# Optimization experiments

Measured on AMD Instinct MI355X. Metric: run time of the kernel, lower is better.

The kernel has to match this reference:

```python
import jax, jax.numpy as jnp
import numpy as np

B, L, N, M, E_EDGE, C = 8, 256, 1024, 8, 16384, 50
EMB, D, TDIM, ETYPES = 768, 256, 50, 50
H, DH, LAYERS = 4, 64, 2
VOCAB_W, VOCAB_E = 30000, 100000
K_SPLIT = N // 2  # fixed kg/logic node split (original uses data-dependent index)


def setup_inputs() -> dict:
    key = jax.random.key(0)
    ks = jax.random.split(key, 32)
    s = 0.02
    inp = {}
    inp["sentence"] = jax.random.randint(ks[0], (B, L), 0, VOCAB_W)
    inp["mask"] = jnp.ones((B, L), jnp.float32)
    inp["nodes"] = jax.random.randint(ks[1], (B, N, M), 0, VOCAB_E)
    inp["node_mask"] = jnp.ones((B, N, M), jnp.float32)
    inp["node_types"] = jax.random.randint(ks[2], (B, N + 1), 0, 100)
    inp["edges"] = jax.random.randint(ks[3], (B, 2, E_EDGE), 0, N + 1)
    inp["edge_types"] = jax.random.randint(ks[4], (B, E_EDGE), 0, ETYPES)
    inp["word_embed"] = jax.random.normal(ks[5], (VOCAB_W, EMB)) * s
    inp["entity_table"] = jax.random.normal(ks[6], (VOCAB_E, EMB)) * s
    inp["type_table"] = jax.random.normal(ks[7], (100, TDIM)) * s
    inp["mlp_w1"] = jax.random.normal(ks[8], (EMB, 1024)) * s
    inp["mlp_b1"] = jnp.zeros((1024,), jnp.float32)
    inp["mlp_w2"] = jax.random.normal(ks[9], (1024, EMB)) * s
    inp["mlp_b2"] = jnp.zeros((EMB,), jnp.float32)
    inp["ntw_w"] = jax.random.normal(ks[10], (EMB, EMB)) * s
    inp["proj_w"] = jax.random.normal(ks[11], (EMB, D)) * s
    inp["proj_b"] = jnp.zeros((D,), jnp.float32)
    inp["type_proj_w"] = jax.random.normal(ks[12], (TDIM, D)) * s
    inp["edge_type_table"] = jax.random.normal(ks[13], (ETYPES, TDIM)) * s
    inp["gnn_wq"] = jax.random.normal(ks[14], (LAYERS, D, D)) * s
    inp["gnn_wk"] = jax.random.normal(ks[15], (LAYERS, D, D)) * s
    inp["gnn_wv"] = jax.random.normal(ks[16], (LAYERS, D, D)) * s
    inp["gnn_we"] = jax.random.normal(ks[17], (LAYERS, TDIM, D)) * s
    inp["cls_w"] = jax.random.normal(ks[18], (EMB + 2 * D, EMB)) * s
    inp["cls_b"] = jnp.zeros((EMB,), jnp.float32)
    inp["cls2_w"] = jax.random.normal(ks[19], (C, EMB)) * s
    inp["cls2_b"] = jnp.zeros((C,), jnp.float32)
    return inp


def reference(sentence, mask, nodes, node_mask, node_types, edges, edge_types,
              word_embed, entity_table, type_table, mlp_w1, mlp_b1, mlp_w2, mlp_b2,
              ntw_w, proj_w, proj_b, type_proj_w, edge_type_table,
              gnn_wq, gnn_wk, gnn_wv, gnn_we, cls_w, cls_b, cls2_w, cls2_b):
    # PLM encoder stand-in: masked mean pool over word embeddings -> [B, EMB]
    text_vec = (word_embed[sentence] * mask[:, :, None]).sum(1) / (mask.sum(1, keepdims=True) + 1e-9)

    def per_graph(nd, nm, nt, eg, et, tv):
        ne = entity_table[nd]                                        # [N, M, EMB]
        logic = jnp.maximum(ne[K_SPLIT:] @ mlp_w1 + mlp_b1, 0.0) @ mlp_w2 + mlp_b2
        ne = jnp.concatenate([ne[:K_SPLIT], logic], axis=0)
        ne = ne @ ntw_w                                              # x @ W (no bias, no transpose)
        ne = (ne * nm[:, :, None]).sum(axis=1)                       # masked sum pool -> [N, EMB]
        h = jnp.concatenate([tv[None], ne], axis=0) @ proj_w + proj_b  # [N+1, D]
        h = h + type_table[nt] @ type_proj_w                         # inject node-type embeds
        src, dst = eg[0], eg[1]
        eemb = edge_type_table[et]                                   # [E, TDIM]
        Nn = N + 1
        for l in range(LAYERS):
            q = (h @ gnn_wq[l]).reshape(Nn, H, DH)
            k = (h @ gnn_wk[l]).reshape(Nn, H, DH)
            v = (h @ gnn_wv[l]).reshape(Nn, H, DH)
            ke = (eemb @ gnn_we[l]).reshape(E_EDGE, H, DH)
            logits = (q[dst] * (k[src] + ke)).sum(-1) / np.float32(np.sqrt(DH))  # [E, H]
            mx = jax.ops.segment_max(logits, dst, num_segments=Nn)
            ex = jnp.exp(logits - mx[dst])
            den = jax.ops.segment_sum(ex, dst, num_segments=Nn)
            alpha = ex / (den[dst] + 1e-9)
            agg = jax.ops.segment_sum(alpha[..., None] * v[src], dst, num_segments=Nn).reshape(Nn, D)
            h = jax.nn.relu(h + agg)
        return h[0], h[1:1 + C]

    ctx, lab = jax.vmap(per_graph)(nodes, node_mask, node_types, edges, edge_types, text_vec)
    ans_t = jnp.broadcast_to(ctx[:, None, :], (B, C, D))
    prompt = jnp.broadcast_to(text_vec[:, None, :], (B, C, EMB))
    pool = jnp.concatenate([ans_t, lab, prompt], axis=2) @ cls_w + cls_b   # [B, C, EMB]
    return (pool * cls2_w[None]).sum(-1) + cls2_b[None]                     # [B, C]
```

## Files before the change

### kernel.cpp

```cpp
#include <hip/hip_runtime.h>
#include <hip/hip_bf16.h>
#include <stdint.h>

using bf16 = __hip_bfloat16;
typedef __attribute__((ext_vector_type(8))) short short8;
typedef __attribute__((ext_vector_type(4))) float f32x4;
typedef __attribute__((address_space(3))) unsigned int lds_u32;
typedef const __attribute__((address_space(1))) unsigned int gbl_u32;

#define HSTRIDE 1040
#define NNODES 1025
#define EE 16384
#define MAXDEG 192

__device__ __forceinline__ bf16 f2b(float x) { return __float2bfloat16(x); }
__device__ __forceinline__ float b2f(bf16 x) { return __bfloat162float(x); }
__device__ __forceinline__ float bu2f(unsigned short u) {
    union { unsigned int i; float f; } x;
    x.i = ((unsigned int)u) << 16;
    return x.f;
}

__device__ __forceinline__ size_t midx(int row) {
    int G = row >> 3, m = row & 7, b = G >> 9;
    return (size_t)(G + 512 * (b + 1)) * 8 + m;
}

__global__ __launch_bounds__(256) void k_transpose_cvt(const float* __restrict__ in,
                                                       bf16* __restrict__ out, int R, int C) {
    __shared__ float tile[32][33];
    int bx = blockIdx.x * 32;
    int by = blockIdx.y * 32;
    int tx = threadIdx.x, ty = threadIdx.y;
    for (int i = 0; i < 32; i += 8)
        tile[ty + i][tx] = in[(size_t)(by + ty + i) * C + bx + tx];
    __syncthreads();
    for (int i = 0; i < 32; i += 8)
        out[(size_t)(bx + ty + i) * R + by + tx] = f2b(tile[tx][ty + i]);
}

__global__ __launch_bounds__(256) void k_transpose_qkv(const float* __restrict__ wq,
                                                       const float* __restrict__ wk,
                                                       const float* __restrict__ wv,
                                                       bf16* __restrict__ out) {
    __shared__ float tile[32][33];
    int z = blockIdx.z;
    int l = z / 3, which = z % 3;
    const float* in = (which == 0 ? wq : which == 1 ? wk : wv) + (size_t)l * 65536;
    bf16* o = out + (size_t)l * 196608 + (size_t)which * 65536;
    int bx = blockIdx.x * 32;
    int by = blockIdx.y * 32;
    int tx = threadIdx.x, ty = threadIdx.y;
    for (int i = 0; i < 32; i += 8)
        tile[ty + i][tx] = in[(size_t)(by + ty + i) * 256 + bx + tx];
    __syncthreads();
    for (int i = 0; i < 32; i += 8)
        o[(size_t)(bx + ty + i) * 256 + by + tx] = f2b(tile[tx][ty + i]);
}

__global__ __launch_bounds__(256) void k_small3(const float* __restrict__ type_table,
                                                const float* __restrict__ type_proj_w,
                                                const float* __restrict__ edge_tt,
                                                const float* __restrict__ gnn_we,
                                                float* __restrict__ tpe,
                                                float* __restrict__ etewe) {
    int r = blockIdx.x, c = threadIdx.x;
    const float* X;
    const float* W;
    float* out;
    if (r < 100) {
        X = type_table + r * 50; W = type_proj_w; out = tpe + r * 256;
    } else if (r < 150) {
        X = edge_tt + (r - 100) * 50; W = gnn_we; out = etewe + (r - 100) * 256;
    } else {
        X = edge_tt + (r - 150) * 50; W = gnn_we + 12800; out = etewe + 12800 + (r - 150) * 256;
    }
    float acc = 0.f;
    for (int k = 0; k < 50; k++) acc += X[k] * W[k * 256 + c];
    out[c] = acc;
}

__global__ __launch_bounds__(256) void k_weff(const float* __restrict__ cls_w,
                                              const float* __restrict__ cls2_w,
                                              const float* __restrict__ cls_b,
                                              const float* __restrict__ cls2_b,
                                              float* __restrict__ weff,
                                              float* __restrict__ beff) {
    int c = blockIdx.y;
    int wave = threadIdx.x >> 6, lane = threadIdx.x & 63;
    int k = blockIdx.x * 4 + wave;
    float acc = 0.f;
    for (int e = lane; e < 768; e += 64)
        acc += cls_w[(size_t)k * 768 + e] * cls2_w[c * 768 + e];
    for (int s = 32; s > 0; s >>= 1) acc += __shfl_xor(acc, s, 64);
    if (lane == 0) weff[c * 1280 + k] = acc;
    if (blockIdx.x == 0 && wave == 0) {
        float bacc = 0.f;
        for (int e = lane; e < 768; e += 64) bacc += cls_b[e] * cls2_w[c * 768 + e];
        for (int s = 32; s > 0; s >>= 1) bacc += __shfl_xor(bacc, s, 64);
        if (lane == 0) beff[c] = bacc + cls2_b[c];
    }
}

__global__ __launch_bounds__(256) void k_textvec_part(const int* __restrict__ sent,
                                                      const float* __restrict__ mask,
                                                      const float* __restrict__ we,
                                                      float* __restrict__ tvp,
                                                      float* __restrict__ msump) {
    int b = blockIdx.x, ch = blockIdx.y, tid = threadIdx.x;
    float a0 = 0.f, a1 = 0.f, a2 = 0.f, ms = 0.f;
    for (int l = ch * 32; l < ch * 32 + 32; l++) {
        int w = sent[b * 256 + l];
        float mm = mask[b * 256 + l];
        const float* row = we + (size_t)w * 768;
        a0 += mm * row[tid];
        a1 += mm * row[tid + 256];
        a2 += mm * row[tid + 512];
        ms += mm;
    }
    float* dst = tvp + (size_t)(b * 8 + ch) * 768;
    dst[tid] = a0;
    dst[tid + 256] = a1;
    dst[tid + 512] = a2;
    if (tid == 0) msump[b * 8 + ch] = ms;
}

__global__ __launch_bounds__(256) void k_tvred(const float* __restrict__ tvp,
                                               const float* __restrict__ msump,
                                               float* __restrict__ tv) {
    int b = blockIdx.x, tid = threadIdx.x;
    float ms = 0.f;
    for (int p = 0; p < 8; p++) ms += msump[b * 8 + p];
    float inv = 1.f / (ms + 1e-9f);
    float a0 = 0.f, a1 = 0.f, a2 = 0.f;
    for (int p = 0; p < 8; p++) {
        const float* s = tvp + (size_t)(b * 8 + p) * 768;
        a0 += s[tid];
        a1 += s[tid + 256];
        a2 += s[tid + 512];
    }
    tv[b * 768 + tid] = a0 * inv;
    tv[b * 768 + tid + 256] = a1 * inv;
    tv[b * 768 + tid + 512] = a2 * inv;
}

__global__ __launch_bounds__(256) void gemm_mlp1(const int* __restrict__ nodes,
                                                 const float* __restrict__ ent,
                                                 const bf16* __restrict__ Bt,
                                                 const float* __restrict__ b1,
                                                 const float* __restrict__ node_mask,
                                                 bf16* __restrict__ pooledh) {
    __shared__ bf16 As[128][32];
    __shared__ bf16 Bs[128][32];
    const int tid = threadIdx.x;
    const int bid = blockIdx.x;
    const int j = bid >> 3;
    const int m0 = (((bid & 7) * 32) + (j >> 3)) << 7;
    const int n0 = (j & 7) << 7;
    const int lane = tid & 63;
    const int wave = tid >> 6;
    const int wm = (wave >> 1) << 6;
    const int wn = (wave & 1) << 6;
    const int rsel = lane & 15;
    const int qd = lane >> 4;
    const int K = 768;

    const float* arow[4];
    int rl_row = tid >> 3;
    int piece4 = (tid & 7) << 2;
#pragma unroll
    for (int p = 0; p < 4; p++) {
        int grow = m0 + p * 32 + rl_row;
        int id = nodes[midx(grow)];
        arow[p] = ent + (size_t)id * 768 + piece4;
    }

    f32x4 acc[4][4];
#pragma unroll
    for (int i = 0; i < 4; i++)
#pragma unroll
        for (int jj = 0; jj < 4; jj++) acc[i][jj] = (f32x4){0.f, 0.f, 0.f, 0.f};

    const int c0 = tid, r0 = c0 >> 2, kk0 = (c0 & 3) << 3;
    const int c1 = tid + 256, r1 = c1 >> 2, kk1 = (c1 & 3) << 3;

    for (int k0 = 0; k0 < K; k0 += 32) {
        __syncthreads();
        const bf16* gb0 = Bt + (size_t)(n0 + r0) * K + (k0 + kk0);
        __builtin_amdgcn_global_load_lds((gbl_u32*)gb0, (lds_u32*)&Bs[r0][kk0], 16, 0, 0);
        const bf16* gb1 = Bt + (size_t)(n0 + r1) * K + (k0 + kk1);
        __builtin_amdgcn_global_load_lds((gbl_u32*)gb1, (lds_u32*)&Bs[r1][kk1], 16, 0, 0);
#pragma unroll
        for (int p = 0; p < 4; p++) {
            float4 v = *(const float4*)(arow[p] + k0);
            union { bf16 h[4]; uint2 u; } pk;
            pk.h[0] = f2b(v.x); pk.h[1] = f2b(v.y); pk.h[2] = f2b(v.z); pk.h[3] = f2b(v.w);
            *(uint2*)&As[p * 32 + rl_row][piece4] = pk.u;
        }
        __syncthreads();
        short8 af[4], bfr[4];
#pragma unroll
        for (int i = 0; i < 4; i++) af[i] = *(const short8*)&As[wm + i * 16 + rsel][qd << 3];
#pragma unroll
        for (int jj = 0; jj < 4; jj++) bfr[jj] = *(const short8*)&Bs[wn + jj * 16 + rsel][qd << 3];
#pragma unroll
        for (int i = 0; i < 4; i++)
#pragma unroll
            for (int jj = 0; jj < 4; jj++)
                acc[i][jj] = __builtin_amdgcn_mfma_f32_16x16x32_bf16(af[i], bfr[jj], acc[i][jj], 0, 0, 0);
    }
#pragma unroll
    for (int i = 0; i < 4; i++) {
        const int rbase = m0 + wm + i * 16 + (qd << 2);
        float w4[4];
#pragma unroll
        for (int r = 0; r < 4; r++) w4[r] = node_mask[midx(rbase + r)];
        const int Gout = (m0 + wm + i * 16 + ((qd & 2) << 2)) >> 3;
#pragma unroll
        for (int jj = 0; jj < 4; jj++) {
            const int col = n0 + wn + jj * 16 + rsel;
            const float bv = b1[col];
            float s = 0.f;
#pragma unroll
            for (int r = 0; r < 4; r++) s += w4[r] * fmaxf(acc[i][jj][r] + bv, 0.f);
            s += __shfl_xor(s, 16, 64);
            if ((qd & 1) == 0) pooledh[(size_t)Gout * 1024 + col] = f2b(s);
        }
    }
}

__global__ __launch_bounds__(256) void k_summask(const float* __restrict__ node_mask,
                                                 float* __restrict__ summask) {
    int G = blockIdx.x * 256 + threadIdx.x;
    if (G >= 4096) return;
    int b = G >> 9;
    const float* p = node_mask + (size_t)(G + 512 * (b + 1)) * 8;
    float s = 0.f;
    for (int m = 0; m < 8; m++) s += p[m];
    summask[G] = s;
}

template <int EPIL>
__global__ __launch_bounds__(256) void gemm_bt(const bf16* __restrict__ A,
                                               const bf16* __restrict__ Bt,
                                               bf16* __restrict__ Cb, float* __restrict__ Cf,
                                               const float* __restrict__ bias,
                                               const float* __restrict__ smr,
                                               int M, int N, int K, int NT, int swz) {
    __shared__ bf16 As[128][32];
    __shared__ bf16 Bs[128][32];
    const int tid = threadIdx.x;
    const int bid = blockIdx.x;
    int mt, nt;
    if (swz) {
        const int MT8 = (M >> 7) >> 3;
        const int j = bid >> 3;
        mt = (bid & 7) * MT8 + j / NT;
        nt = j - (j / NT) * NT;
    } else {
        mt = bid / NT;
        nt = bid - mt * NT;
    }
    const int m0 = mt << 7;
    const int n0 = nt << 7;
    const int lane = tid & 63;
    const int wave = tid >> 6;
    const int wm = (wave >> 1) << 6;
    const int wn = (wave & 1) << 6;
    const int rsel = lane & 15;
    const int qd = lane >> 4;
    f32x4 acc[4][4];
#pragma unroll
    for (int i = 0; i < 4; i++)
#pragma unroll
        for (int jj = 0; jj < 4; jj++) acc[i][jj] = (f32x4){0.f, 0.f, 0.f, 0.f};
// ... 35 lines not shown
        }
#pragma unroll
        for (int jj = 0; jj < 4; jj++) {
            const int col = n0 + wn + jj * 16 + rsel;
            float bv = 0.f;
            if constexpr (EPIL == 4 || EPIL == 5) bv = bias[col];
#pragma unroll
            for (int r = 0; r < 4; r++) {
                const int row = rbase + r;
                if constexpr (EPIL == 0) {
                    Cb[(size_t)row * N + col] = f2b(acc[i][jj][r]);
                } else if constexpr (EPIL == 4) {
                    const int bb = row >> 10, nn2 = row & 1023;
                    Cf[((size_t)bb * HSTRIDE + 1 + nn2) * 256 + col] = acc[i][jj][r] + bv;
                } else {
                    const int dest = row + 512 * ((row >> 9) + 1);
                    Cb[(size_t)dest * N + col] = f2b(acc[i][jj][r] + sm4[r] * bv);
                }
            }
        }
    }
}

__global__ __launch_bounds__(256) void k_pool_kg(const int* __restrict__ nodes,
                                                 const float* __restrict__ nmask,
                                                 const float* __restrict__ ent,
                                                 bf16* __restrict__ pooled) {
    int bid = blockIdx.x;
    int b = bid >> 9, n = bid & 511;
    int tid = threadIdx.x;
    int base = (((b << 10) + n) << 3);
    float a0 = 0.f, a1 = 0.f, a2 = 0.f;
    for (int m = 0; m < 8; m++) {
        float w = nmask[base + m];
        const float* row = ent + (size_t)nodes[base + m] * 768;
        a0 += w * row[tid];
        a1 += w * row[tid + 256];
        a2 += w * row[tid + 512];
    }
    bf16* dst = pooled + (size_t)((b << 10) + n) * 768;
    dst[tid] = f2b(a0);
    dst[tid + 256] = f2b(a1);
    dst[tid + 512] = f2b(a2);
}

__global__ __launch_bounds__(256) void k_tpe_add(const int* __restrict__ ntypes,
                                                 const float* __restrict__ tpe,
                                                 const float* __restrict__ tv,
                                                 const float* __restrict__ proj_w,
                                                 const float* __restrict__ proj_b,
                                                 float* __restrict__ h, bf16* __restrict__ hbf) {
    int i = blockIdx.x;
    int b = blockIdx.y;
    int c = threadIdx.x;
    size_t idx = ((size_t)b * HSTRIDE + i) * 256 + c;
    if (i < NNODES) {
        int t = ntypes[b * NNODES + i];
        float v;
        if (i == 0) {
            v = proj_b[c];
            for (int k = 0; k < 768; k++) v += tv[b * 768 + k] * proj_w[k * 256 + c];
        } else {
            v = h[idx];
        }
        v += tpe[t * 256 + c];
        h[idx] = v;
        hbf[idx] = f2b(v);
    } else {
        h[idx] = 0.f;
        hbf[idx] = f2b(0.f);
    }
}

__global__ void k_zero(int* p, int n) {
    int i = blockIdx.x * 256 + threadIdx.x;
    if (i < n) p[i] = 0;
}

__global__ __launch_bounds__(256) void k_count(const int* __restrict__ edges,
                                               int* __restrict__ counts) {
    int flat = blockIdx.x * 256 + threadIdx.x;
    int b = flat >> 14, e = flat & (EE - 1);
    int d = edges[b * 2 * EE + EE + e];
    atomicAdd(&counts[b * NNODES + d], 1);
}

__global__ __launch_bounds__(256) void k_scan(const int* __restrict__ counts,
                                              int* __restrict__ offs, int* __restrict__ cursor) {
    int b = blockIdx.x, t = threadIdx.x;
    __shared__ int tsum[256];
    int beg = t * 5;
    int end = beg + 5;
    if (end > NNODES) end = NNODES;
    int cl[5];
    int s = 0;
    for (int i = beg; i < end; i++) {
        int v = counts[b * NNODES + i];
        cl[i - beg] = v;
        s += v;
    }
    tsum[t] = s;
    __syncthreads();
    for (int d = 1; d < 256; d <<= 1) {
        int v = tsum[t];
        int vo = (t >= d) ? tsum[t - d] : 0;
        __syncthreads();
        tsum[t] = v + vo;
        __syncthreads();
    }
    int run = (t == 0) ? 0 : tsum[t - 1];
    for (int i = beg; i < end; i++) {
        offs[b * 1026 + i] = run;
        cursor[b * NNODES + i] = run;
        run += cl[i - beg];
    }
    if (beg == NNODES) offs[b * 1026 + NNODES] = run;
}

__global__ __launch_bounds__(256) void k_scatter(const int* __restrict__ edges,
                                                 int* __restrict__ cursor, int* __restrict__ eord) {
    int flat = blockIdx.x * 256 + threadIdx.x;
    int b = flat >> 14, e = flat & (EE - 1);
    int d = edges[b * 2 * EE + EE + e];
    int pos = atomicAdd(&cursor[b * NNODES + d], 1);
    eord[b * EE + pos] = e;
}

__global__ __launch_bounds__(256) void k_gnn_node(const int* __restrict__ edges,
                                                  const int* __restrict__ etypes,
                                                  const int* __restrict__ offs,
                                                  const int* __restrict__ eord,
                                                  const float* __restrict__ etewe,
                                                  const bf16* __restrict__ qkv,
                                                  float* __restrict__ h, bf16* __restrict__ hbf) {
    int bid = blockIdx.x;
    int b = bid / NNODES, n = bid % NNODES;
    int o0 = offs[b * 1026 + n];
    int deg = offs[b * 1026 + n + 1] - o0;
    if (deg > MAXDEG) deg = MAXDEG;
    int tid = threadIdx.x, lane = tid & 63, wave = tid >> 6;
    __shared__ float qs[256];
    __shared__ float elog[MAXDEG][4];
    __shared__ int srcs[MAXDEG];
    __shared__ float smax[4], sden[4];
    __shared__ float vpart[4][256];
    size_t qbase = ((size_t)(b * HSTRIDE + n)) * 768;
    qs[tid] = b2f(qkv[qbase + tid]);
    __syncthreads();
// ... 19 lines not shown
    __syncthreads();
    if (deg > 0) {
        int hh = wave;
        float m = -1e30f;
        for (int i = lane; i < deg; i += 64) m = fmaxf(m, elog[i][hh]);
        for (int s = 32; s > 0; s >>= 1) m = fmaxf(m, __shfl_xor(m, s, 64));
        float den = 0.f;
        for (int i = lane; i < deg; i += 64) den += expf(elog[i][hh] - m);
        for (int s = 32; s > 0; s >>= 1) den += __shfl_xor(den, s, 64);
        if (lane == 0) { smax[hh] = m; sden[hh] = den; }
    }
    __syncthreads();
    for (int i = tid; i < deg; i += 256) {
#pragma unroll
        for (int hh = 0; hh < 4; hh++)
            elog[i][hh] = expf(elog[i][hh] - smax[hh]) / (sden[hh] + 1e-9f);
    }
    __syncthreads();
    float a0 = 0.f, a1 = 0.f, a2 = 0.f, a3 = 0.f;
    const int hsel = lane >> 4;
    for (int i = wave; i < deg; i += 4) {
        float w = elog[i][hsel];
        const bf16* vrow = qkv + ((size_t)(b * HSTRIDE + srcs[i])) * 768 + 512 + lane * 4;
        ushort4 u = *reinterpret_cast<const ushort4*>(vrow);
        a0 += w * bu2f(u.x);
        a1 += w * bu2f(u.y);
        a2 += w * bu2f(u.z);
        a3 += w * bu2f(u.w);
    }
    vpart[wave][lane * 4 + 0] = a0;
    vpart[wave][lane * 4 + 1] = a1;
    vpart[wave][lane * 4 + 2] = a2;
    vpart[wave][lane * 4 + 3] = a3;
    __syncthreads();
    float acc = vpart[0][tid] + vpart[1][tid] + vpart[2][tid] + vpart[3][tid];
    size_t hidx = ((size_t)(b * HSTRIDE + n)) * 256 + tid;
    float v = fmaxf(h[hidx] + acc, 0.f);
    h[hidx] = v;
    hbf[hidx] = f2b(v);
}

__global__ __launch_bounds__(256) void k_cls(const float* __restrict__ h,
                                             const float* __restrict__ tv,
                                             const float* __restrict__ weff,
                                             const float* __restrict__ beff,
                                             float* __restrict__ out) {
    int bc = blockIdx.x;
    int b = bc / 50, c = bc % 50;
    int tid = threadIdx.x;
    const float* we = weff + c * 1280;
    float acc = 0.f;
// ... 35 lines not shown
    const float* ntw_w        = (const float*)d_in[14];
    const float* proj_w       = (const float*)d_in[15];
    const float* proj_b       = (const float*)d_in[16];
    const float* type_proj_w  = (const float*)d_in[17];
    const float* edge_tt      = (const float*)d_in[18];
    const float* gnn_wq       = (const float*)d_in[19];
    const float* gnn_wk       = (const float*)d_in[20];
    const float* gnn_wv       = (const float*)d_in[21];
    const float* gnn_we       = (const float*)d_in[22];
    const float* cls_w        = (const float*)d_in[23];
    const float* cls_b        = (const float*)d_in[24];
    const float* cls2_w       = (const float*)d_in[25];
    const float* cls2_b       = (const float*)d_in[26];

    char* ws = (char*)d_ws;
    size_t off = 0;
    auto alloc = [&](size_t bytes) {
        size_t r = off;
        off += (bytes + 255) & ~((size_t)255);
        return r;
    };
    bf16* w1t     = (bf16*)(ws + alloc((size_t)1024 * 768 * 2));
    bf16* w2t     = (bf16*)(ws + alloc((size_t)768 * 1024 * 2));
    bf16* ntwt    = (bf16*)(ws + alloc((size_t)768 * 768 * 2));
    bf16* projt   = (bf16*)(ws + alloc((size_t)256 * 768 * 2));
    bf16* wqkvt   = (bf16*)(ws + alloc((size_t)2 * 768 * 256 * 2));
    float* tpe    = (float*)(ws + alloc((size_t)100 * 256 * 4));
    float* etewe  = (float*)(ws + alloc((size_t)2 * 50 * 256 * 4));
    float* weff   = (float*)(ws + alloc((size_t)50 * 1280 * 4));
    float* beff   = (float*)(ws + alloc(256));
    float* tv     = (float*)(ws + alloc((size_t)8 * 768 * 4));
    float* tvp    = (float*)(ws + alloc((size_t)64 * 768 * 4));
    float* msump  = (float*)(ws + alloc((size_t)64 * 4));
    float* summask= (float*)(ws + alloc((size_t)4096 * 4));
    int* counts   = (int*)(ws + alloc((size_t)8 * NNODES * 4));
    int* offs     = (int*)(ws + alloc((size_t)8 * 1026 * 4));
    int* cursor   = (int*)(ws + alloc((size_t)8 * NNODES * 4));
    int* eord     = (int*)(ws + alloc((size_t)8 * EE * 4));
    bf16* pooledh = (bf16*)(ws + alloc((size_t)4096 * 1024 * 2));
    bf16* pooled  = (bf16*)(ws + alloc((size_t)8192 * 768 * 2));
    bf16* ne2     = (bf16*)(ws + alloc((size_t)8192 * 768 * 2));
    float* h      = (float*)(ws + alloc((size_t)8 * HSTRIDE * 256 * 4));
    bf16* hbf     = (bf16*)(ws + alloc((size_t)8 * HSTRIDE * 256 * 2));
    bf16* qkv     = (bf16*)(ws + alloc((size_t)8 * HSTRIDE * 768 * 2));

    dim3 tb(32, 8);
    k_transpose_cvt<<<dim3(32, 24), tb, 0, stream>>>(mlp_w1, w1t, 768, 1024);
    k_transpose_cvt<<<dim3(24, 32), tb, 0, stream>>>(mlp_w2, w2t, 1024, 768);
    k_transpose_cvt<<<dim3(24, 24), tb, 0, stream>>>(ntw_w, ntwt, 768, 768);
    k_transpose_cvt<<<dim3(8, 24), tb, 0, stream>>>(proj_w, projt, 768, 256);
    k_transpose_qkv<<<dim3(8, 8, 6), tb, 0, stream>>>(gnn_wq, gnn_wk, gnn_wv, wqkvt);
    k_small3<<<200, 256, 0, stream>>>(type_table, type_proj_w, edge_tt, gnn_we, tpe, etewe);
    k_weff<<<dim3(320, 50), 256, 0, stream>>>(cls_w, cls2_w, cls_b, cls2_b, weff, beff);
    k_textvec_part<<<dim3(8, 8), 256, 0, stream>>>(sentence, mask, word_embed, tvp, msump);
    k_tvred<<<8, 256, 0, stream>>>(tvp, msump, tv);

    gemm_mlp1<<<2048, 256, 0, stream>>>(nodes, entity_table, w1t, mlp_b1, node_mask, pooledh);
    k_summask<<<16, 256, 0, stream>>>(node_mask, summask);
    gemm_bt<5><<<192, 256, 0, stream>>>(pooledh, w2t, pooled, nullptr, mlp_b2, summask, 4096, 768, 1024, 6, 1);
    k_pool_kg<<<4096, 256, 0, stream>>>(nodes, node_mask, entity_table, pooled);
    gemm_bt<0><<<384, 256, 0, stream>>>(pooled, ntwt, ne2, nullptr, nullptr, nullptr, 8192, 768, 768, 6, 1);
    gemm_bt<4><<<128, 256, 0, stream>>>(ne2, projt, nullptr, h, proj_b, nullptr, 8192, 256, 768, 2, 1);
    k_tpe_add<<<dim3(1040, 8), 256, 0, stream>>>(node_types, tpe, tv, proj_w, proj_b, h, hbf);

    k_zero<<<(8 * NNODES + 255) / 256, 256, 0, stream>>>(counts, 8 * NNODES);
    k_count<<<512, 256, 0, stream>>>(edges, counts);
    k_scan<<<8, 256, 0, stream>>>(counts, offs, cursor);
    k_scatter<<<512, 256, 0, stream>>>(edges, cursor, eord);

    for (int l = 0; l < 2; l++) {
        gemm_bt<0><<<390, 256, 0, stream>>>(hbf, wqkvt + l * 196608, qkv, nullptr, nullptr, nullptr, 8320, 768, 256, 6, 0);
        k_gnn_node<<<8 * NNODES, 256, 0, stream>>>(edges, edge_types, offs, eord,
                                                   etewe + l * 12800, qkv, h, hbf);
    }
    k_cls<<<400, 256, 0, stream>>>(h, tv, weff, beff, (float*)d_out);
}
```

Measured before the change: 870.4 us.

## Merge prep kernels into mega-launches and fold ntw into proj weight

Replaces about 17 small launches (weight transposes, table projections, text-vector reduction, edge counting, scan and scatter) with a few multi-role kernels that dispatch on block index. The two chained GEMMs (pooled@ntw then @proj) are precomputed as one combined 768x256 weight, removing the 8192x768x768 GEMM and its intermediate buffer. The text-vector projection is split into partial sums reduced in k_tpe_add. This cuts launch overhead and FLOPs. The cost is heterogeneous blocks inside each launch, plus a small rounding change from multiplying the weights before casting to bf16.

```diff
diff --git a/kernel.cpp b/kernel.cpp
--- a/kernel.cpp
+++ b/kernel.cpp
@@ -26,231 +26,15 @@
     return (size_t)(G + 512 * (b + 1)) * 8 + m;
 }
 
-__global__ __launch_bounds__(256) void k_transpose_cvt(const float* __restrict__ in,
-                                                       bf16* __restrict__ out, int R, int C) {
-    __shared__ float tile[32][33];
-    int bx = blockIdx.x * 32;
-    int by = blockIdx.y * 32;
-    int tx = threadIdx.x, ty = threadIdx.y;
-    for (int i = 0; i < 32; i += 8)
-        tile[ty + i][tx] = in[(size_t)(by + ty + i) * C + bx + tx];
-    __syncthreads();
-    for (int i = 0; i < 32; i += 8)
-        out[(size_t)(bx + ty + i) * R + by + tx] = f2b(tile[tx][ty + i]);
-}
-
-__global__ __launch_bounds__(256) void k_transpose_qkv(const float* __restrict__ wq,
-                                                       const float* __restrict__ wk,
-                                                       const float* __restrict__ wv,
-                                                       bf16* __restrict__ out) {
-    __shared__ float tile[32][33];
-    int z = blockIdx.z;
-    int l = z / 3, which = z % 3;
-    const float* in = (which == 0 ? wq : which == 1 ? wk : wv) + (size_t)l * 65536;
-    bf16* o = out + (size_t)l * 196608 + (size_t)which * 65536;
-    int bx = blockIdx.x * 32;
-    int by = blockIdx.y * 32;
-    int tx = threadIdx.x, ty = threadIdx.y;
-    for (int i = 0; i < 32; i += 8)
-        tile[ty + i][tx] = in[(size_t)(by + ty + i) * 256 + bx + tx];
-    __syncthreads();
-    for (int i = 0; i < 32; i += 8)
-        o[(size_t)(bx + ty + i) * 256 + by + tx] = f2b(tile[tx][ty + i]);
-}
-
-__global__ __launch_bounds__(256) void k_small3(const float* __restrict__ type_table,
-                                                const float* __restrict__ type_proj_w,
-                                                const float* __restrict__ edge_tt,
-                                                const float* __restrict__ gnn_we,
-                                                float* __restrict__ tpe,
-                                                float* __restrict__ etewe) {
-    int r = blockIdx.x, c = threadIdx.x;
-    const float* X;
-    const float* W;
-    float* out;
-    if (r < 100) {
-        X = type_table + r * 50; W = type_proj_w; out = tpe + r * 256;
-    } else if (r < 150) {
-        X = edge_tt + (r - 100) * 50; W = gnn_we; out = etewe + (r - 100) * 256;
-    } else {
-        X = edge_tt + (r - 150) * 50; W = gnn_we + 12800; out = etewe + 12800 + (r - 150) * 256;
-    }
-    float acc = 0.f;
-    for (int k = 0; k < 50; k++) acc += X[k] * W[k * 256 + c];
-    out[c] = acc;
-}
-
-__global__ __launch_bounds__(256) void k_weff(const float* __restrict__ cls_w,
-                                              const float* __restrict__ cls2_w,
-                                              const float* __restrict__ cls_b,
-                                              const float* __restrict__ cls2_b,
-                                              float* __restrict__ weff,
-                                              float* __restrict__ beff) {
-    int c = blockIdx.y;
-    int wave = threadIdx.x >> 6, lane = threadIdx.x & 63;
-    int k = blockIdx.x * 4 + wave;
-    float acc = 0.f;
-    for (int e = lane; e < 768; e += 64)
-        acc += cls_w[(size_t)k * 768 + e] * cls2_w[c * 768 + e];
-    for (int s = 32; s > 0; s >>= 1) acc += __shfl_xor(acc, s, 64);
-    if (lane == 0) weff[c * 1280 + k] = acc;
-    if (blockIdx.x == 0 && wave == 0) {
-        float bacc = 0.f;
-        for (int e = lane; e < 768; e += 64) bacc += cls_b[e] * cls2_w[c * 768 + e];
-        for (int s = 32; s > 0; s >>= 1) bacc += __shfl_xor(bacc, s, 64);
-        if (lane == 0) beff[c] = bacc + cls2_b[c];
-    }
-}
-
-__global__ __launch_bounds__(256) void k_textvec_part(const int* __restrict__ sent,
-                                                      const float* __restrict__ mask,
-                                                      const float* __restrict__ we,
-                                                      float* __restrict__ tvp,
-                                                      float* __restrict__ msump) {
-    int b = blockIdx.x, ch = blockIdx.y, tid = threadIdx.x;
-    float a0 = 0.f, a1 = 0.f, a2 = 0.f, ms = 0.f;
-    for (int l = ch * 32; l < ch * 32 + 32; l++) {
-        int w = sent[b * 256 + l];
-        float mm = mask[b * 256 + l];
-        const float* row = we + (size_t)w * 768;
-        a0 += mm * row[tid];
-        a1 += mm * row[tid + 256];
-        a2 += mm * row[tid + 512];
-        ms += mm;
-    }
-    float* dst = tvp + (size_t)(b * 8 + ch) * 768;
-    dst[tid] = a0;
-    dst[tid + 256] = a1;
-    dst[tid + 512] = a2;
-    if (tid == 0) msump[b * 8 + ch] = ms;
-}
-
-__global__ __launch_bounds__(256) void k_tvred(const float* __restrict__ tvp,
-                                               const float* __restrict__ msump,
-                                               float* __restrict__ tv) {
-    int b = blockIdx.x, tid = threadIdx.x;
-    float ms = 0.f;
-    for (int p = 0; p < 8; p++) ms += msump[b * 8 + p];
-    float inv = 1.f / (ms + 1e-9f);
-    float a0 = 0.f, a1 = 0.f, a2 = 0.f;
-    for (int p = 0; p < 8; p++) {
-        const float* s = tvp + (size_t)(b * 8 + p) * 768;
-        a0 += s[tid];
-        a1 += s[tid + 256];
-        a2 += s[tid + 512];
-    }
-    tv[b * 768 + tid] = a0 * inv;
-    tv[b * 768 + tid + 256] = a1 * inv;
-    tv[b * 768 + tid + 512] = a2 * inv;
-}
-
-__global__ __launch_bounds__(256) void gemm_mlp1(const int* __restrict__ nodes,
-                                                 const float* __restrict__ ent,
-                                                 const bf16* __restrict__ Bt,
-                                                 const float* __restrict__ b1,
-                                                 const float* __restrict__ node_mask,
-                                                 bf16* __restrict__ pooledh) {
+template <int EPIL>
+__device__ __forceinline__ void gemm_body(const bf16* __restrict__ A, const bf16* __restrict__ Bt,
+                                          bf16* __restrict__ Cb, float* __restrict__ Cf,
+                                          const float* __restrict__ bias,
+                                          const float* __restrict__ smr,
+                                          int M, int N, int K, int NT, int swz, int bid) {
     __shared__ bf16 As[128][32];
     __shared__ bf16 Bs[128][32];
     const int tid = threadIdx.x;
-    const int bid = blockIdx.x;
-    const int j = bid >> 3;
-    const int m0 = (((bid & 7) * 32) + (j >> 3)) << 7;
-    const int n0 = (j & 7) << 7;
-    const int lane = tid & 63;
-    const int wave = tid >> 6;
-    const int wm = (wave >> 1) << 6;
-    const int wn = (wave & 1) << 6;
-    const int rsel = lane & 15;
-    const int qd = lane >> 4;
-    const int K = 768;
-
-    const float* arow[4];
-    int rl_row = tid >> 3;
-    int piece4 = (tid & 7) << 2;
-#pragma unroll
-    for (int p = 0; p < 4; p++) {
-        int grow = m0 + p * 32 + rl_row;
-        int id = nodes[midx(grow)];
-        arow[p] = ent + (size_t)id * 768 + piece4;
-    }
-
-    f32x4 acc[4][4];
-#pragma unroll
-    for (int i = 0; i < 4; i++)
-#pragma unroll
-        for (int jj = 0; jj < 4; jj++) acc[i][jj] = (f32x4){0.f, 0.f, 0.f, 0.f};
-
-    const int c0 = tid, r0 = c0 >> 2, kk0 = (c0 & 3) << 3;
-    const int c1 = tid + 256, r1 = c1 >> 2, kk1 = (c1 & 3) << 3;
-
-    for (int k0 = 0; k0 < K; k0 += 32) {
-        __syncthreads();
-        const bf16* gb0 = Bt + (size_t)(n0 + r0) * K + (k0 + kk0);
-        __builtin_amdgcn_global_load_lds((gbl_u32*)gb0, (lds_u32*)&Bs[r0][kk0], 16, 0, 0);
-        const bf16* gb1 = Bt + (size_t)(n0 + r1) * K + (k0 + kk1);
-        __builtin_amdgcn_global_load_lds((gbl_u32*)gb1, (lds_u32*)&Bs[r1][kk1], 16, 0, 0);
-#pragma unroll
-        for (int p = 0; p < 4; p++) {
-            float4 v = *(const float4*)(arow[p] + k0);
-            union { bf16 h[4]; uint2 u; } pk;
-            pk.h[0] = f2b(v.x); pk.h[1] = f2b(v.y); pk.h[2] = f2b(v.z); pk.h[3] = f2b(v.w);
-            *(uint2*)&As[p * 32 + rl_row][piece4] = pk.u;
-        }
-        __syncthreads();
-        short8 af[4], bfr[4];
-#pragma unroll
-        for (int i = 0; i < 4; i++) af[i] = *(const short8*)&As[wm + i * 16 + rsel][qd << 3];
-#pragma unroll
-        for (int jj = 0; jj < 4; jj++) bfr[jj] = *(const short8*)&Bs[wn + jj * 16 + rsel][qd << 3];
-#pragma unroll
-        for (int i = 0; i < 4; i++)
-#pragma unroll
-            for (int jj = 0; jj < 4; jj++)
-                acc[i][jj] = __builtin_amdgcn_mfma_f32_16x16x32_bf16(af[i], bfr[jj], acc[i][jj], 0, 0, 0);
-    }
-#pragma unroll
-    for (int i = 0; i < 4; i++) {
-        const int rbase = m0 + wm + i * 16 + (qd << 2);
-        float w4[4];
-#pragma unroll
-        for (int r = 0; r < 4; r++) w4[r] = node_mask[midx(rbase + r)];
-        const int Gout = (m0 + wm + i * 16 + ((qd & 2) << 2)) >> 3;
-#pragma unroll
-        for (int jj = 0; jj < 4; jj++) {
-            const int col = n0 + wn + jj * 16 + rsel;
-            const float bv = b1[col];
-            float s = 0.f;
-#pragma unroll
-            for (int r = 0; r < 4; r++) s += w4[r] * fmaxf(acc[i][jj][r] + bv, 0.f);
-            s += __shfl_xor(s, 16, 64);
-            if ((qd & 1) == 0) pooledh[(size_t)Gout * 1024 + col] = f2b(s);
-        }
-    }
-}
-
-__global__ __launch_bounds__(256) void k_summask(const float* __restrict__ node_mask,
-                                                 float* __restrict__ summask) {
-    int G = blockIdx.x * 256 + threadIdx.x;
-    if (G >= 4096) return;
-    int b = G >> 9;
-    const float* p = node_mask + (size_t)(G + 512 * (b + 1)) * 8;
-    float s = 0.f;
-    for (int m = 0; m < 8; m++) s += p[m];
-    summask[G] = s;
-}
-
-template <int EPIL>
-__global__ __launch_bounds__(256) void gemm_bt(const bf16* __restrict__ A,
-                                               const bf16* __restrict__ Bt,
-                                               bf16* __restrict__ Cb, float* __restrict__ Cf,
-                                               const float* __restrict__ bias,
-                                               const float* __restrict__ smr,
-                                               int M, int N, int K, int NT, int swz) {
-    __shared__ bf16 As[128][32];
-    __shared__ bf16 Bs[128][32];
-    const int tid = threadIdx.x;
-    const int bid = blockIdx.x;
     int mt, nt;
     if (swz) {
         const int MT8 = (M >> 7) >> 3;
@@ -332,32 +116,380 @@
     }
 }
 
-__global__ __launch_bounds__(256) void k_pool_kg(const int* __restrict__ nodes,
-                                                 const float* __restrict__ nmask,
-                                                 const float* __restrict__ ent,
-                                                 bf16* __restrict__ pooled) {
-    int bid = blockIdx.x;
-    int b = bid >> 9, n = bid & 511;
+template <int EPIL>
+__global__ __launch_bounds__(256) void gemm_bt(const bf16* __restrict__ A,
+                                               const bf16* __restrict__ Bt,
+                                               bf16* __restrict__ Cb, float* __restrict__ Cf,
+                                               const float* __restrict__ bias,
+                                               const float* __restrict__ smr,
+                                               int M, int N, int K, int NT, int swz) {
+    gemm_body<EPIL>(A, Bt, Cb, Cf, bias, smr, M, N, K, NT, swz, blockIdx.x);
+}
+
+__device__ __forceinline__ void tr_tile(const float* __restrict__ in, bf16* __restrict__ out,
+                                        int R, int C, int gx, int gy, int tid,
+                                        float (*tile)[33]) {
+    int tx = tid & 31, ty = tid >> 5;
+    int bx = gx * 32, by = gy * 32;
+    for (int i = 0; i < 32; i += 8)
+        tile[ty + i][tx] = in[(size_t)(by + ty + i) * C + bx + tx];
+    __syncthreads();
+    for (int i = 0; i < 32; i += 8)
+        out[(size_t)(bx + ty + i) * R + by + tx] = f2b(tile[tx][ty + i]);
+}
+
+__global__ __launch_bounds__(256) void k_prep(
+    const float* __restrict__ mlp_w1, const float* __restrict__ mlp_w2,
+    const float* __restrict__ ntw_w, const float* __restrict__ proj_w,
+    const float* __restrict__ gnn_wq, const float* __restrict__ gnn_wk,
+    const float* __restrict__ gnn_wv,
+    const float* __restrict__ type_table, const float* __restrict__ type_proj_w,
+    const float* __restrict__ edge_tt, const float* __restrict__ gnn_we,
+    const float* __restrict__ cls_w, const float* __restrict__ cls2_w,
+    const float* __restrict__ cls_b, const float* __restrict__ cls2_b,
+    const int* __restrict__ sent, const float* __restrict__ maskp,
+    const float* __restrict__ we,
+    bf16* __restrict__ w1t, bf16* __restrict__ w2t, bf16* __restrict__ ntwbf,
+    bf16* __restrict__ projt, bf16* __restrict__ wqkvt,
+    float* __restrict__ tpe, float* __restrict__ etewe,
+    float* __restrict__ weff, float* __restrict__ beff,
+    float* __restrict__ tvp, float* __restrict__ msump, int* __restrict__ counts) {
+    __shared__ float tile[32][33];
+    int u = blockIdx.x;
     int tid = threadIdx.x;
-    int base = (((b << 10) + n) << 3);
-    float a0 = 0.f, a1 = 0.f, a2 = 0.f;
-    for (int m = 0; m < 8; m++) {
-        float w = nmask[base + m];
-        const float* row = ent + (size_t)nodes[base + m] * 768;
-        a0 += w * row[tid];
-        a1 += w * row[tid + 256];
-        a2 += w * row[tid + 512];
-    }
-    bf16* dst = pooled + (size_t)((b << 10) + n) * 768;
-    dst[tid] = f2b(a0);
-    dst[tid + 256] = f2b(a1);
-    dst[tid + 512] = f2b(a2);
+    if (u < 768) {
+        tr_tile(mlp_w1, w1t, 768, 1024, u % 32, u / 32, tid, tile);
+        return;
+    }
+    u -= 768;
+    if (u < 768) {
+        tr_tile(mlp_w2, w2t, 1024, 768, u % 24, u / 24, tid, tile);
+        return;
+    }
+    u -= 768;
+    if (u < 576) {
+        int base = (u * 256 + tid) * 4;
+        float4 v = *(const float4*)(ntw_w + base);
+        union { bf16 h[4]; uint2 q; } pk;
+        pk.h[0] = f2b(v.x); pk.h[1] = f2b(v.y); pk.h[2] = f2b(v.z); pk.h[3] = f2b(v.w);
+        *(uint2*)(ntwbf + base) = pk.q;
+        return;
+    }
+    u -= 576;
+    if (u < 192) {
+        tr_tile(proj_w, projt, 768, 256, u % 8, u / 8, tid, tile);
+        return;
+    }
+    u -= 192;
+    if (u < 384) {
+        int z = u / 64, v = u % 64;
+        int l = z / 3, which = z % 3;
+        const float* in = (which == 0 ? gnn_wq : which == 1 ? gnn_wk : gnn_wv) + (size_t)l * 65536;
+        bf16* o = wqkvt + (size_t)l * 196608 + (size_t)which * 65536;
+        tr_tile(in, o, 256, 256, v % 8, v / 8, tid, tile);
+        return;
+    }
+    u -= 384;
+    if (u < 200) {
+        const float* X;
+        const float* W;
+        float* out;
+        if (u < 100) {
+            X = type_table + u * 50; W = type_proj_w; out = tpe + u * 256;
+        } else if (u < 150) {
+            X = edge_tt + (u - 100) * 50; W = gnn_we; out = etewe + (u - 100) * 256;
+        } else {
+            X = edge_tt + (u - 150) * 50; W = gnn_we + 12800; out = etewe + 12800 + (u - 150) * 256;
+        }
+        float acc = 0.f;
+        for (int k = 0; k < 50; k++) acc += X[k] * W[k * 256 + tid];
+        out[tid] = acc;
+        return;
+    }
+    u -= 200;
+    if (u < 320) {
+        int wave = tid >> 6, lane = tid & 63;
+        int k = u * 4 + wave;
+        float wrow[12];
+#pragma unroll
+        for (int t = 0; t < 12; t++) wrow[t] = cls_w[(size_t)k * 768 + t * 64 + lane];
+        for (int c = 0; c < 50; c++) {
+            const float* c2 = cls2_w + c * 768;
+            float acc = 0.f;
+#pragma unroll
+            for (int t = 0; t < 12; t++) acc += wrow[t] * c2[t * 64 + lane];
+            for (int s = 32; s > 0; s >>= 1) acc += __shfl_xor(acc, s, 64);
+            if (lane == 0) weff[c * 1280 + k] = acc;
+        }
+        if (u == 0) {
+            float brow[12];
+#pragma unroll
+            for (int t = 0; t < 12; t++) brow[t] = cls_b[t * 64 + lane];
+            for (int c = wave; c < 50; c += 4) {
+                const float* c2 = cls2_w + c * 768;
+                float acc = 0.f;
+#pragma unroll
+                for (int t = 0; t < 12; t++) acc += brow[t] * c2[t * 64 + lane];
+                for (int s = 32; s > 0; s >>= 1) acc += __shfl_xor(acc, s, 64);
+                if (lane == 0) beff[c] = acc + cls2_b[c];
+            }
+        }
+        return;
+    }
+    u -= 320;
+    if (u < 64) {
+        int b = u >> 3, ch = u & 7;
+        float a0 = 0.f, a1 = 0.f, a2 = 0.f, ms = 0.f;
+        for (int l = ch * 32; l < ch * 32 + 32; l++) {
+            int w = sent[b * 256 + l];
+            float mm = maskp[b * 256 + l];
+            const float* row = we + (size_t)w * 768;
+            a0 += mm * row[tid];
+            a1 += mm * row[tid + 256];
+            a2 += mm * row[tid + 512];
+            ms += mm;
+        }
+        float* dst = tvp + (size_t)(b * 8 + ch) * 768;
+        dst[tid] = a0;
+        dst[tid + 256] = a1;
+        dst[tid + 512] = a2;
+        if (tid == 0) msump[b * 8 + ch] = ms;
+        return;
+    }
+    u -= 64;
+    {
+        int i = u * 256 + tid;
+        if (i < 8 * NNODES) counts[i] = 0;
+    }
+}
+
+__global__ __launch_bounds__(256) void k_mid(
+    const bf16* __restrict__ projt, const bf16* __restrict__ ntwbf, bf16* __restrict__ wnpt,
+    const float* __restrict__ tvp, const float* __restrict__ msump, float* __restrict__ tv,
+    const float* __restrict__ node_mask, float* __restrict__ summask,
+    const int* __restrict__ edges, int* __restrict__ counts) {
+    int u = blockIdx.x;
+    int tid = threadIdx.x;
+    if (u < 12) {
+        gemm_body<0>(projt, ntwbf, wnpt, nullptr, nullptr, nullptr, 256, 768, 768, 6, 0, u);
+        return;
+    }
+    u -= 12;
+    if (u < 8) {
+        int b = u;
+        float ms = 0.f;
+        for (int p = 0; p < 8; p++) ms += msump[b * 8 + p];
+        float inv = 1.f / (ms + 1e-9f);
+        float a0 = 0.f, a1 = 0.f, a2 = 0.f;
+        for (int p = 0; p < 8; p++) {
+            const float* s = tvp + (size_t)(b * 8 + p) * 768;
+            a0 += s[tid];
+            a1 += s[tid + 256];
+            a2 += s[tid + 512];
+        }
+        tv[b * 768 + tid] = a0 * inv;
+        tv[b * 768 + tid + 256] = a1 * inv;
+        tv[b * 768 + tid + 512] = a2 * inv;
+        return;
+    }
+    u -= 8;
+    if (u < 16) {
+        int G = u * 256 + tid;
+        if (G < 4096) {
+            int b = G >> 9;
+            const float* p = node_mask + (size_t)(G + 512 * (b + 1)) * 8;
+            float s = 0.f;
+            for (int m = 0; m < 8; m++) s += p[m];
+            summask[G] = s;
+        }
+        return;
+    }
+    u -= 16;
+    {
+        int flat = u * 256 + tid;
+        int b = flat >> 14, e = flat & (EE - 1);
+        int d = edges[b * 2 * EE + EE + e];
+        atomicAdd(&counts[b * NNODES + d], 1);
+    }
+}
+
+__global__ __launch_bounds__(256) void k_mlp1_scan(
+    const int* __restrict__ nodes, const float* __restrict__ ent,
+    const bf16* __restrict__ Bt, const float* __restrict__ b1,
+    const float* __restrict__ node_mask, bf16* __restrict__ pooledh,
+    const int* __restrict__ counts, int* __restrict__ offs, int* __restrict__ cursor) {
+    __shared__ bf16 As[128][32];
+    __shared__ bf16 Bs[128][32];
+    __shared__ int tsum[256];
+    const int tid = threadIdx.x;
+    const int bid = blockIdx.x;
+    if (bid >= 2048) {
+        int b = bid - 2048, t = tid;
+        int beg = t * 5;
+        int end = beg + 5;
+        if (end > NNODES) end = NNODES;
+        int cl[5];
+        int s = 0;
+        for (int i = beg; i < end; i++) {
+            int v = counts[b * NNODES + i];
+            cl[i - beg] = v;
+            s += v;
+        }
+        tsum[t] = s;
+        __syncthreads();
+        for (int d = 1; d < 256; d <<= 1) {
+            int v = tsum[t];
+            int vo = (t >= d) ? tsum[t - d] : 0;
+            __syncthreads();
+            tsum[t] = v + vo;
+            __syncthreads();
+        }
+        int run = (t == 0) ? 0 : tsum[t - 1];
+        for (int i = beg; i < end; i++) {
+            offs[b * 1026 + i] = run;
+            cursor[b * NNODES + i] = run;
+            run += cl[i - beg];
+        }
+        if (beg == NNODES) offs[b * 1026 + NNODES] = run;
+        return;
+    }
+    const int j = bid >> 3;
+    const int m0 = (((bid & 7) * 32) + (j >> 3)) << 7;
+    const int n0 = (j & 7) << 7;
+    const int lane = tid & 63;
+    const int wave = tid >> 6;
+    const int wm = (wave >> 1) << 6;
+    const int wn = (wave & 1) << 6;
+    const int rsel = lane & 15;
+    const int qd = lane >> 4;
+    const int K = 768;
+
+    const float* arow[4];
+    int rl_row = tid >> 3;
+    int piece4 = (tid & 7) << 2;
+#pragma unroll
+    for (int p = 0; p < 4; p++) {
+        int grow = m0 + p * 32 + rl_row;
+        int id = nodes[midx(grow)];
+        arow[p] = ent + (size_t)id * 768 + piece4;
+    }
+
+    f32x4 acc[4][4];
+#pragma unroll
+    for (int i = 0; i < 4; i++)
+#pragma unroll
+        for (int jj = 0; jj < 4; jj++) acc[i][jj] = (f32x4){0.f, 0.f, 0.f, 0.f};
+
+    const int c0 = tid, r0 = c0 >> 2, kk0 = (c0 & 3) << 3;
+    const int c1 = tid + 256, r1 = c1 >> 2, kk1 = (c1 & 3) << 3;
+
+    for (int k0 = 0; k0 < K; k0 += 32) {
+        __syncthreads();
+        const bf16* gb0 = Bt + (size_t)(n0 + r0) * K + (k0 + kk0);
+        __builtin_amdgcn_global_load_lds((gbl_u32*)gb0, (lds_u32*)&Bs[r0][kk0], 16, 0, 0);
+        const bf16* gb1 = Bt + (size_t)(n0 + r1) * K + (k0 + kk1);
+        __builtin_amdgcn_global_load_lds((gbl_u32*)gb1, (lds_u32*)&Bs[r1][kk1], 16, 0, 0);
+#pragma unroll
+        for (int p = 0; p < 4; p++) {
+            float4 v = *(const float4*)(arow[p] + k0);
+            union { bf16 h[4]; uint2 u; } pk;
+            pk.h[0] = f2b(v.x); pk.h[1] = f2b(v.y); pk.h[2] = f2b(v.z); pk.h[3] = f2b(v.w);
+            *(uint2*)&As[p * 32 + rl_row][piece4] = pk.u;
+        }
+        __syncthreads();
+        short8 af[4], bfr[4];
+#pragma unroll
+        for (int i = 0; i < 4; i++) af[i] = *(const short8*)&As[wm + i * 16 + rsel][qd << 3];
+#pragma unroll
+        for (int jj = 0; jj < 4; jj++) bfr[jj] = *(const short8*)&Bs[wn + jj * 16 + rsel][qd << 3];
+#pragma unroll
+        for (int i = 0; i < 4; i++)
+#pragma unroll
+            for (int jj = 0; jj < 4; jj++)
+                acc[i][jj] = __builtin_amdgcn_mfma_f32_16x16x32_bf16(af[i], bfr[jj], acc[i][jj], 0, 0, 0);
+    }
+#pragma unroll
+    for (int i = 0; i < 4; i++) {
+        const int rbase = m0 + wm + i * 16 + (qd << 2);
+        float w4[4];
+#pragma unroll
+        for (int r = 0; r < 4; r++) w4[r] = node_mask[midx(rbase + r)];
+        const int Gout = (m0 + wm + i * 16 + ((qd & 2) << 2)) >> 3;
+#pragma unroll
+        for (int jj = 0; jj < 4; jj++) {
+            const int col = n0 + wn + jj * 16 + rsel;
+            const float bv = b1[col];
+            float s = 0.f;
+#pragma unroll
+            for (int r = 0; r < 4; r++) s += w4[r] * fmaxf(acc[i][jj][r] + bv, 0.f);
+            s += __shfl_xor(s, 16, 64);
+            if ((qd & 1) == 0) pooledh[(size_t)Gout * 1024 + col] = f2b(s);
+        }
+    }
+}
+
+__global__ __launch_bounds__(256) void k_mega4(
+    const bf16* __restrict__ pooledh, const bf16* __restrict__ w2t, bf16* __restrict__ pooled,
+    const float* __restrict__ mlp_b2, const float* __restrict__ summask,
+    const int* __restrict__ nodes, const float* __restrict__ nmask, const float* __restrict__ ent,
+    const float* __restrict__ tv, const float* __restrict__ proj_w, float* __restrict__ hp) {
+    int u = blockIdx.x;
+    int tid = threadIdx.x;
+    if (u < 192) {
+        gemm_body<5>(pooledh, w2t, pooled, nullptr, mlp_b2, summask, 4096, 768, 1024, 6, 1, u);
+        return;
+    }
+    u -= 192;
+    if (u < 4096) {
+        int b = u >> 9, n = u & 511;
+        int base = (((b << 10) + n) << 3);
+        float a0 = 0.f, a1 = 0.f, a2 = 0.f;
+        for (int m = 0; m < 8; m++) {
+            float w = nmask[base + m];
+            const float* row = ent + (size_t)nodes[base + m] * 768;
+            a0 += w * row[tid];
+            a1 += w * row[tid + 256];
+            a2 += w * row[tid + 512];
+        }
+        bf16* dst = pooled + (size_t)((b << 10) + n) * 768;
+        dst[tid] = f2b(a0);
+        dst[tid + 256] = f2b(a1);
+        dst[tid + 512] = f2b(a2);
+        return;
+    }
+    u -= 4096;
+    {
+        int b = u / 6, kc = u % 6;
+        float acc = 0.f;
+        for (int k = kc * 128; k < kc * 128 + 128; k++)
+            acc += tv[b * 768 + k] * proj_w[k * 256 + tid];
+        hp[(size_t)(b * 6 + kc) * 256 + tid] = acc;
+    }
+}
+
+__global__ __launch_bounds__(256) void k_mega5(
+    const bf16* __restrict__ pooled, const bf16* __restrict__ wnpt,
+    float* __restrict__ h, const float* __restrict__ proj_b,
+    const int* __restrict__ edges, int* __restrict__ cursor, int* __restrict__ eord) {
+    int u = blockIdx.x;
+    int tid = threadIdx.x;
+    if (u < 128) {
+        gemm_body<4>(pooled, wnpt, nullptr, h, proj_b, nullptr, 8192, 256, 768, 2, 1, u);
+        return;
+    }
+    u -= 128;
+    {
+        int flat = u * 256 + tid;
+        int b = flat >> 14, e = flat & (EE - 1);
+        int d = edges[b * 2 * EE + EE + e];
+        int pos = atomicAdd(&cursor[b * NNODES + d], 1);
+        eord[b * EE + pos] = e;
+    }
 }
 
 __global__ __launch_bounds__(256) void k_tpe_add(const int* __restrict__ ntypes,
                                                  const float* __restrict__ tpe,
-                                                 const float* __restrict__ tv,
-                                                 const float* __restrict__ proj_w,
+                                                 const float* __restrict__ hp,
                                                  const float* __restrict__ proj_b,
                                                  float* __restrict__ h, bf16* __restrict__ hbf) {
     int i = blockIdx.x;
@@ -369,7 +501,7 @@
         float v;
         if (i == 0) {
             v = proj_b[c];
-            for (int k = 0; k < 768; k++) v += tv[b * 768 + k] * proj_w[k * 256 + c];
+            for (int p = 0; p < 6; p++) v += hp[(size_t)(b * 6 + p) * 256 + c];
         } else {
             v = h[idx];
         }
@@ -380,60 +512,6 @@
         h[idx] = 0.f;
         hbf[idx] = f2b(0.f);
     }
-}
-
-__global__ void k_zero(int* p, int n) {
-    int i = blockIdx.x * 256 + threadIdx.x;
-    if (i < n) p[i] = 0;
-}
-
-__global__ __launch_bounds__(256) void k_count(const int* __restrict__ edges,
-                                               int* __restrict__ counts) {
-    int flat = blockIdx.x * 256 + threadIdx.x;
-    int b = flat >> 14, e = flat & (EE - 1);
-    int d = edges[b * 2 * EE + EE + e];
-    atomicAdd(&counts[b * NNODES + d], 1);
-}
-
-__global__ __launch_bounds__(256) void k_scan(const int* __restrict__ counts,
-                                              int* __restrict__ offs, int* __restrict__ cursor) {
-    int b = blockIdx.x, t = threadIdx.x;
-    __shared__ int tsum[256];
-    int beg = t * 5;
-    int end = beg + 5;
-    if (end > NNODES) end = NNODES;
-    int cl[5];
-    int s = 0;
-    for (int i = beg; i < end; i++) {
-        int v = counts[b * NNODES + i];
-        cl[i - beg] = v;
-        s += v;
-    }
-    tsum[t] = s;
-    __syncthreads();
-    for (int d = 1; d < 256; d <<= 1) {
-        int v = tsum[t];
-        int vo = (t >= d) ? tsum[t - d] : 0;
-        __syncthreads();
-        tsum[t] = v + vo;
-        __syncthreads();
-    }
-    int run = (t == 0) ? 0 : tsum[t - 1];
-    for (int i = beg; i < end; i++) {
-        offs[b * 1026 + i] = run;
-        cursor[b * NNODES + i] = run;
-        run += cl[i - beg];
-    }
-    if (beg == NNODES) offs[b * 1026 + NNODES] = run;
-}
-
-__global__ __launch_bounds__(256) void k_scatter(const int* __restrict__ edges,
-                                                 int* __restrict__ cursor, int* __restrict__ eord) {
-    int flat = blockIdx.x * 256 + threadIdx.x;
-    int b = flat >> 14, e = flat & (EE - 1);
-    int d = edges[b * 2 * EE + EE + e];
-    int pos = atomicAdd(&cursor[b * NNODES + d], 1);
-    eord[b * EE + pos] = e;
 }
 
 __global__ __launch_bounds__(256) void k_gnn_node(const int* __restrict__ edges,
@@ -499,11 +577,11 @@
     for (int i = wave; i < deg; i += 4) {
         float w = elog[i][hsel];
         const bf16* vrow = qkv + ((size_t)(b * HSTRIDE + srcs[i])) * 768 + 512 + lane * 4;
-        ushort4 u = *reinterpret_cast<const ushort4*>(vrow);
-        a0 += w * bu2f(u.x);
-        a1 += w * bu2f(u.y);
-        a2 += w * bu2f(u.z);
-        a3 += w * bu2f(u.w);
+        ushort4 uu = *reinterpret_cast<const ushort4*>(vrow);
+        a0 += w * bu2f(uu.x);
+        a1 += w * bu2f(uu.y);
+        a2 += w * bu2f(uu.z);
+        a3 += w * bu2f(uu.w);
     }
     vpart[wave][lane * 4 + 0] = a0;
     vpart[wave][lane * 4 + 1] = a1;
@@ -585,8 +663,9 @@
     };
     bf16* w1t     = (bf16*)(ws + alloc((size_t)1024 * 768 * 2));
     bf16* w2t     = (bf16*)(ws + alloc((size_t)768 * 1024 * 2));
-    bf16* ntwt    = (bf16*)(ws + alloc((size_t)768 * 768 * 2));
+    bf16* ntwbf   = (bf16*)(ws + alloc((size_t)768 * 768 * 2));
     bf16* projt   = (bf16*)(ws + alloc((size_t)256 * 768 * 2));
+    bf16* wnpt    = (bf16*)(ws + alloc((size_t)256 * 768 * 2));
     bf16* wqkvt   = (bf16*)(ws + alloc((size_t)2 * 768 * 256 * 2));
     float* tpe    = (float*)(ws + alloc((size_t)100 * 256 * 4));
     float* etewe  = (float*)(ws + alloc((size_t)2 * 50 * 256 * 4));
@@ -595,6 +674,7 @@
     float* tv     = (float*)(ws + alloc((size_t)8 * 768 * 4));
     float* tvp    = (float*)(ws + alloc((size_t)64 * 768 * 4));
     float* msump  = (float*)(ws + alloc((size_t)64 * 4));
+    float* hp     = (float*)(ws + alloc((size_t)48 * 256 * 4));
     float* summask= (float*)(ws + alloc((size_t)4096 * 4));
     int* counts   = (int*)(ws + alloc((size_t)8 * NNODES * 4));
     int* offs     = (int*)(ws + alloc((size_t)8 * 1026 * 4));
@@ -602,37 +682,28 @@
     int* eord     = (int*)(ws + alloc((size_t)8 * EE * 4));
     bf16* pooledh = (bf16*)(ws + alloc((size_t)4096 * 1024 * 2));
     bf16* pooled  = (bf16*)(ws + alloc((size_t)8192 * 768 * 2));
-    bf16* ne2     = (bf16*)(ws + alloc((size_t)8192 * 768 * 2));
     float* h      = (float*)(ws + alloc((size_t)8 * HSTRIDE * 256 * 4));
     bf16* hbf     = (bf16*)(ws + alloc((size_t)8 * HSTRIDE * 256 * 2));
     bf16* qkv     = (bf16*)(ws + alloc((size_t)8 * HSTRIDE * 768 * 2));
 
-    dim3 tb(32, 8);
-    k_transpose_cvt<<<dim3(32, 24), tb, 0, stream>>>(mlp_w1, w1t, 768, 1024);
-    k_transpose_cvt<<<dim3(24, 32), tb, 0, stream>>>(mlp_w2, w2t, 1024, 768);
-    k_transpose_cvt<<<dim3(24, 24), tb, 0, stream>>>(ntw_w, ntwt, 768, 768);
-    k_transpose_cvt<<<dim3(8, 24), tb, 0, stream>>>(proj_w, projt, 768, 256);
-    k_transpose_qkv<<<dim3(8, 8, 6), tb, 0, stream>>>(gnn_wq, gnn_wk, gnn_wv, wqkvt);
-    k_small3<<<200, 256, 0, stream>>>(type_table, type_proj_w, edge_tt, gnn_we, tpe, etewe);
-    k_weff<<<dim3(320, 50), 256, 0, stream>>>(cls_w, cls2_w, cls_b, cls2_b, weff, beff);
-    k_textvec_part<<<dim3(8, 8), 256, 0, stream>>>(sentence, mask, word_embed, tvp, msump);
-    k_tvred<<<8, 256, 0, stream>>>(tvp, msump, tv);
-
-    gemm_mlp1<<<2048, 256, 0, stream>>>(nodes, entity_table, w1t, mlp_b1, node_mask, pooledh);
-    k_summask<<<16, 256, 0, stream>>>(node_mask, summask);
-    gemm_bt<5><<<192, 256, 0, stream>>>(pooledh, w2t, pooled, nullptr, mlp_b2, summask, 4096, 768, 1024, 6, 1);
-    k_pool_kg<<<4096, 256, 0, stream>>>(nodes, node_mask, entity_table, pooled);
-    gemm_bt<0><<<384, 256, 0, stream>>>(pooled, ntwt, ne2, nullptr, nullptr, nullptr, 8192, 768, 768, 6, 1);
-    gemm_bt<4><<<128, 256, 0, stream>>>(ne2, projt, nullptr, h, proj_b, nullptr, 8192, 256, 768, 2, 1);
-    k_tpe_add<<<dim3(1040, 8), 256, 0, stream>>>(node_types, tpe, tv, proj_w, proj_b, h, hbf);
-
-    k_zero<<<(8 * NNODES + 255) / 256, 256, 0, stream>>>(counts, 8 * NNODES);
-    k_count<<<512, 256, 0, stream>>>(edges, counts);
-    k_scan<<<8, 256, 0, stream>>>(counts, offs, cursor);
-    k_scatter<<<512, 256, 0, stream>>>(edges, cursor, eord);
+    k_prep<<<3305, 256, 0, stream>>>(mlp_w1, mlp_w2, ntw_w, proj_w, gnn_wq, gnn_wk, gnn_wv,
+                                     type_table, type_proj_w, edge_tt, gnn_we,
+                                     cls_w, cls2_w, cls_b, cls2_b,
+                                     sentence, mask, word_embed,
+                                     w1t, w2t, ntwbf, projt, wqkvt,
+                                     tpe, etewe, weff, beff, tvp, msump, counts);
+    k_mid<<<548, 256, 0, stream>>>(projt, ntwbf, wnpt, tvp, msump, tv,
+                                   node_mask, summask, edges, counts);
+    k_mlp1_scan<<<2056, 256, 0, stream>>>(nodes, entity_table, w1t, mlp_b1, node_mask, pooledh,
+                                          counts, offs, cursor);
+    k_mega4<<<4336, 256, 0, stream>>>(pooledh, w2t, pooled, mlp_b2, summask,
+                                      nodes, node_mask, entity_table, tv, proj_w, hp);
+    k_mega5<<<640, 256, 0, stream>>>(pooled, wnpt, h, proj_b, edges, cursor, eord);
+    k_tpe_add<<<dim3(1040, 8), 256, 0, stream>>>(node_types, tpe, hp, proj_b, h, hbf);
 
     for (int l = 0; l < 2; l++) {
-        gemm_bt<0><<<390, 256, 0, stream>>>(hbf, wqkvt + l * 196608, qkv, nullptr, nullptr, nullptr, 8320, 768, 256, 6, 0);
+        gemm_bt<0><<<390, 256, 0, stream>>>(hbf, wqkvt + l * 196608, qkv, nullptr, nullptr,
+                                            nullptr, 8320, 768, 256, 6, 0);
         k_gnn_node<<<8 * NNODES, 256, 0, stream>>>(edges, edge_types, offs, eord,
                                                    etewe + l * 12800, qkv, h, hbf);
     }
```

Result: faster. 804.5 us (-7.6%).
